# Kernel optimization log

Hardware: AMD Instinct MI355X
Metric: run time of the kernel (lower is better)

## Reference

```python
import jax, jax.numpy as jnp
import numpy as np

B_J0 = 0.01
BETA = 1.8   # isAdapt=1
LENS = 0.5
DT = 1.0
IN_SIZE = 1
STRIDE = IN_SIZE
T = 784 // STRIDE
HID = (512, 512, 512)
OUT = 10
N = 256


def _create_general_mask(dim, c_min, c_max, min_dc, max_dc, phase_max, T):
    # faithful port of ASRNN_general.create_general_mask (numpy, static)
    dcs = np.linspace(min_dc, max_dc, dim)
    cycles = np.linspace(c_min, c_max, dim)
    shifts = np.linspace(0.0, float(int(phase_max * c_max)), dim)
    rows = []
    for cyc, dc, ps in zip(cycles, dcs, shifts):
        cyc = int(np.round(cyc))
        on = int(np.round(dc * cyc))
        pat = [1.0] * on + [0.0] * (cyc - on)
        ps = int(np.round(ps))
        if ps > 0:
            pat = pat[-ps:] + pat[:-ps]
        rows.append(pat * (T // cyc) + pat[: T % cyc])
    return np.asarray(rows, dtype=np.float32)  # [dim, T]

MASK1 = jnp.asarray(_create_general_mask(HID[0], 2, 8, 0.2, 0.8, 0.5, T))
MASK2 = jnp.asarray(_create_general_mask(HID[1], 4, 16, 0.2, 0.8, 0.5, T))
MASK3 = jnp.asarray(_create_general_mask(HID[2], 8, 32, 0.2, 0.8, 0.5, T))

# per-step input gather indices (faithful to the start_idx branch in forward)
_starts = np.arange(T) * STRIDE
_IDX = np.where(_starts[:, None] < T - IN_SIZE,
                _starts[:, None] + np.arange(IN_SIZE)[None, :],
                (784 - IN_SIZE) + np.arange(IN_SIZE)[None, :])  # [T, IN]


@jax.custom_vjp
def act_fun(x):
    return (x > 0.0).astype(x.dtype)

def _act_fwd(x):
    return (x > 0.0).astype(x.dtype), x

def _act_bwd(x, g):
    return (g * (jnp.abs(x) < LENS).astype(g.dtype),)

act_fun.defvjp(_act_fwd, _act_bwd)


def _mem_update(inputs, mem, spike, tau_adp, b, tau_m, mask_t):
    alpha = jnp.exp(-DT / tau_m)
    ro = jnp.exp(-DT / tau_adp)
    b_new = ro * b + (1.0 - ro) * spike
    Bth = B_J0 + BETA * b_new
    mem_new = mem * alpha + (1.0 - alpha) * inputs - Bth * spike * DT
    mem_new = jnp.where(mask_t == 0.0, mem, mem_new)
    spike_new = act_fun(mem_new - Bth) * mask_t
    return mem_new, spike_new, b_new


def _forward(x, wi1, bi1, wh1, bh1, wi2, bi2, wh2, bh2, wi3, bi3, wo, bo,
             tau_adp1, tau_adp2, tau_adp3, tau_m1, tau_m2, tau_m3):
    n = x.shape[0]
    x_seq = jnp.transpose(x[:, _IDX], (1, 0, 2))            # [T, N, IN]
    pre1 = jnp.einsum('tni,hi->tnh', x_seq, wi1) + bi1       # [T, N, H1]

    def step_fn(carry, xs):
        mem1, spk1, b1, mem2, spk2, b2, mem3, spk3, b3, out_sum, s1, s2, s3 = carry
        p1, m1, m2, m3 = xs
        h1_in = p1 + spk1 @ wh1.T + bh1
        mem1, spk1, b1 = _mem_update(h1_in, mem1, spk1, tau_adp1, b1, tau_m1, m1)
        h2_in = spk1 @ wi2.T + bi2 + spk2 @ wh2.T + bh2
        mem2, spk2, b2 = _mem_update(h2_in, mem2, spk2, tau_adp2, b2, tau_m2, m2)
        h3_in = spk2 @ wi3.T + bi3
        mem3, spk3, b3 = _mem_update(h3_in, mem3, spk3, tau_adp3, b3, tau_m3, m3)
        out_sum = out_sum + spk3 @ wo.T + bo
        return (mem1, spk1, b1, mem2, spk2, b2, mem3, spk3, b3,
                out_sum, s1 + spk1, s2 + spk2, s3 + spk3), None

    z = lambda h: jnp.zeros((n, h), x.dtype)
    f = lambda h: jnp.full((n, h), B_J0, x.dtype)
    carry0 = (z(HID[0]), z(HID[0]), f(HID[0]),
              z(HID[1]), z(HID[1]), f(HID[1]),
              z(HID[2]), z(HID[2]), f(HID[2]),
              jnp.zeros((n, OUT), x.dtype), z(HID[0]), z(HID[1]), z(HID[2]))
    xs = (pre1, MASK1.T, MASK2.T, MASK3.T)
    carry, _ = jax.lax.scan(step_fn, carry0, xs)
    out_sum, s1, s2, s3 = carry[9], carry[10], carry[11], carry[12]
    outputs = out_sum / T
    layer_fr = jnp.stack([s1.sum() / (n * HID[0] * T),
                          s2.sum() / (n * HID[1] * T),
                          s3.sum() / (n * HID[2] * T)])
    return outputs, s1 / T, s2 / T, s3 / T, layer_fr


def setup_inputs() -> dict:
    key = jax.random.key(0)
    ks = jax.random.split(key, 20)
    def xav(k, shp):
        fan_in, fan_out = shp[1], shp[0]
        s = np.sqrt(2.0 / (fan_in + fan_out))
        return jax.random.normal(k, shp, jnp.float32) * s
    return {
        'x': jax.random.uniform(ks[0], (N, 784), jnp.float32),
        'wi1': xav(ks[1], (HID[0], IN_SIZE)), 'bi1': jnp.zeros((HID[0],), jnp.float32),
        'wh1': xav(ks[2], (HID[0], HID[0])), 'bh1': jnp.zeros((HID[0],), jnp.float32),
        'wi2': xav(ks[3], (HID[1], HID[0])), 'bi2': jnp.zeros((HID[1],), jnp.float32),
        'wh2': xav(ks[4], (HID[1], HID[1])), 'bh2': jnp.zeros((HID[1],), jnp.float32),
        'wi3': xav(ks[5], (HID[2], HID[1])), 'bi3': jnp.zeros((HID[2],), jnp.float32),
        'wo': xav(ks[6], (OUT, HID[2])), 'bo': jnp.zeros((OUT,), jnp.float32),
        'tau_adp1': 700.0 + 25.0 * jax.random.normal(ks[7], (HID[0],), jnp.float32),
        'tau_adp2': 700.0 + 25.0 * jax.random.normal(ks[8], (HID[1],), jnp.float32),
        'tau_adp3': 700.0 + 25.0 * jax.random.normal(ks[9], (HID[2],), jnp.float32),
        'tau_m1': 5.0 + jax.random.normal(ks[10], (HID[0],), jnp.float32),
        'tau_m2': 5.0 + jax.random.normal(ks[11], (HID[1],), jnp.float32),
        'tau_m3': 5.0 + jax.random.normal(ks[12], (HID[2],), jnp.float32),
    }


def reference(x, wi1, bi1, wh1, bh1, wi2, bi2, wh2, bh2, wi3, bi3, wo, bo,
              tau_adp1, tau_adp2, tau_adp3, tau_m1, tau_m2, tau_m3):
    return _forward(x, wi1, bi1, wh1, bh1, wi2, bi2, wh2, bh2, wi3, bi3, wo, bo,
                    tau_adp1, tau_adp2, tau_adp3, tau_m1, tau_m2, tau_m3)
```

## Files before the change

### kernel.cpp

```cpp
#include <hip/hip_runtime.h>
#include <stdint.h>

#pragma clang fp contract(off)


static constexpr int    TS      = 784;
static constexpr size_t WS_WT1  = 0;
static constexpr size_t WS_WT2A = 1u << 20;
static constexpr size_t WS_WT2B = 2u << 20;
static constexpr size_t WS_WT3  = 3u << 20;
static constexpr size_t WS_M1   = 4u << 20;
static constexpr size_t WS_M2   = WS_M1 + (size_t)TS * 512;
static constexpr size_t WS_M3   = WS_M2 + (size_t)TS * 512;
static constexpr size_t WS_FRP  = WS_M3 + (size_t)TS * 512;

__device__ __forceinline__ float exp_np(float x) {
  float q = rintf(x * 1.442695040f);
  float r = __fmaf_rn(-q, 0.693359375f, x);
  r = __fmaf_rn(-q, -2.12194440e-4f, r);
  float r2 = r * r;
  float p = 1.9875691500e-4f;
  p = __fmaf_rn(p, r, 1.3981999507e-3f);
  p = __fmaf_rn(p, r, 8.3334519073e-3f);
  p = __fmaf_rn(p, r, 4.1665795894e-2f);
  p = __fmaf_rn(p, r, 1.6666665459e-1f);
  p = __fmaf_rn(p, r, 5.0000001201e-1f);
  p = __fmaf_rn(p, r2, r);
  p = p + 1.0f;
  return ldexpf(p, (int)q);
}

__device__ __forceinline__ int mask_val(int l, int h, int t) {
  const double cmin = (l == 0) ? 2.0 : ((l == 1) ? 4.0 : 8.0);
  const double cmax = (l == 0) ? 8.0 : ((l == 1) ? 16.0 : 32.0);
  const double smax = (l == 0) ? 4.0 : ((l == 1) ? 8.0 : 16.0);
  const double cD = (cmax - cmin) / 511.0;
  const double dD = (0.8 - 0.2) / 511.0;
  const double sD = smax / 511.0;
  const double hd = (double)h;
  double cycd = (h == 511) ? cmax : __dadd_rn(cmin, __dmul_rn(hd, cD));
  double dcd  = (h == 511) ? 0.8  : __dadd_rn(0.2,  __dmul_rn(hd, dD));
  double psd  = (h == 511) ? smax : __dmul_rn(hd, sD);
  int cyc = __double2int_rn(cycd);
  int on  = __double2int_rn(__dmul_rn(dcd, (double)cyc));
  int ps  = __double2int_rn(psd);
  int eff = (ps >= cyc) ? 0 : ps;
  int pos = (t % cyc) - eff;
  if (pos < 0) pos += cyc;
  return (pos < on) ? 1 : 0;
}

__global__ void setup_masks(char* __restrict__ ws) {
  const int t = blockIdx.x, tid = threadIdx.x;
  uint8_t* m1 = (uint8_t*)(ws + WS_M1);
  uint8_t* m2 = (uint8_t*)(ws + WS_M2);
  uint8_t* m3 = (uint8_t*)(ws + WS_M3);
  for (int h = tid; h < 512; h += 256) {
    m1[t * 512 + h] = (uint8_t)mask_val(0, h, t);
    m2[t * 512 + h] = (uint8_t)mask_val(1, h, t);
    m3[t * 512 + h] = (uint8_t)mask_val(2, h, t);
  }
}

__global__ void transpose_kernel(const float* __restrict__ wh1,
                                 const float* __restrict__ wi2,
                                 const float* __restrict__ wh2,
                                 const float* __restrict__ wi3,
                                 char* __restrict__ ws) {
  const int k = blockIdx.x;
  const int m = blockIdx.y;
  const float* W = (m == 0) ? wh1 : (m == 1) ? wi2 : (m == 2) ? wh2 : wi3;
  float* T = (float*)(ws + (size_t)m * (1u << 20));
  for (int j = threadIdx.x; j < 512; j += 256)
    T[(size_t)k * 512 + j] = W[(size_t)j * 512 + k];
}

__device__ __forceinline__ uint32_t upd32(float hin, uint32_t mk, uint32_t osp,
                                          float al, float om, float r, float omr,
                                          float& memv, float& bv) {
  float t1 = r * bv;
  float bn = osp ? (t1 + omr) : t1;
  float bt = 1.8f * bn;
  float Bth = 0.01f + bt;
  float m1 = memv * al;
  float m2 = om * hin;
  float m3 = m1 + m2;
  float mn = osp ? (m3 - Bth) : m3;
  if (!mk) mn = memv;
  uint32_t sn = (mk && (mn - Bth) > 0.0f) ? 1u : 0u;
  memv = mn; bv = bn;
  return sn;
}

__device__ __forceinline__ int expand_list(const uint64_t* __restrict__ bm,
                                           uint32_t mysp, int h,
                                           ushort* __restrict__ kl) {
  const int wh = h >> 6, bpos = h & 63;
  int cnt = 0, rank = 0;
#pragma unroll
  for (int w = 0; w < 8; ++w) {
    uint64_t v = bm[w];
    int pc = __builtin_popcountll(v);
    if (w < wh) rank += pc;
    cnt += pc;
  }
  rank += __builtin_popcountll(bm[wh] & ((1ull << bpos) - 1ull));
  if (mysp) kl[rank] = (ushort)h;
  return cnt;
}

__device__ __forceinline__ float gather_from(const float* __restrict__ base,
                                             const ushort* kl, int from, int cnt,
                                             float s) {
  int i = from;
  for (; i + 16 <= cnt; i += 16) {
    float w0  = base[(size_t)kl[i + 0]  << 9];
    float w1  = base[(size_t)kl[i + 1]  << 9];
    float w2  = base[(size_t)kl[i + 2]  << 9];
    float w3  = base[(size_t)kl[i + 3]  << 9];
    float w4  = base[(size_t)kl[i + 4]  << 9];
    float w5  = base[(size_t)kl[i + 5]  << 9];
    float w6  = base[(size_t)kl[i + 6]  << 9];
    float w7  = base[(size_t)kl[i + 7]  << 9];
    float w8  = base[(size_t)kl[i + 8]  << 9];
    float w9  = base[(size_t)kl[i + 9]  << 9];
    float w10 = base[(size_t)kl[i + 10] << 9];
    float w11 = base[(size_t)kl[i + 11] << 9];
    float w12 = base[(size_t)kl[i + 12] << 9];
    float w13 = base[(size_t)kl[i + 13] << 9];
    float w14 = base[(size_t)kl[i + 14] << 9];
    float w15 = base[(size_t)kl[i + 15] << 9];
    s = s + w0;  s = s + w1;  s = s + w2;  s = s + w3;
    s = s + w4;  s = s + w5;  s = s + w6;  s = s + w7;
    s = s + w8;  s = s + w9;  s = s + w10; s = s + w11;
    s = s + w12; s = s + w13; s = s + w14; s = s + w15;
  }
  for (; i + 4 <= cnt; i += 4) {
    float w0 = base[(size_t)kl[i + 0] << 9];
    float w1 = base[(size_t)kl[i + 1] << 9];
    float w2 = base[(size_t)kl[i + 2] << 9];
    float w3 = base[(size_t)kl[i + 3] << 9];
    s = s + w0; s = s + w1; s = s + w2; s = s + w3;
  }
  for (; i < cnt; ++i) s = s + base[(size_t)kl[i] << 9];
  return s;
}

__device__ __forceinline__ void dual_gather(
    const float* __restrict__ bA, const ushort* __restrict__ klA, int cntA,
    const float* __restrict__ bB, const ushort* __restrict__ klB, int cntB,
    float& outA, float& outB) {
  float a = 0.0f, b = 0.0f;
  int iA = 0, iB = 0;
  while (iA + 8 <= cntA && iB + 8 <= cntB) {
    float wa0 = bA[(size_t)klA[iA + 0] << 9];
    float wa1 = bA[(size_t)klA[iA + 1] << 9];
    float wa2 = bA[(size_t)klA[iA + 2] << 9];
    float wa3 = bA[(size_t)klA[iA + 3] << 9];
    float wa4 = bA[(size_t)klA[iA + 4] << 9];
    float wa5 = bA[(size_t)klA[iA + 5] << 9];
    float wa6 = bA[(size_t)klA[iA + 6] << 9];
    float wa7 = bA[(size_t)klA[iA + 7] << 9];
    float wb0 = bB[(size_t)klB[iB + 0] << 9];
    float wb1 = bB[(size_t)klB[iB + 1] << 9];
    float wb2 = bB[(size_t)klB[iB + 2] << 9];
    float wb3 = bB[(size_t)klB[iB + 3] << 9];
    float wb4 = bB[(size_t)klB[iB + 4] << 9];
    float wb5 = bB[(size_t)klB[iB + 5] << 9];
    float wb6 = bB[(size_t)klB[iB + 6] << 9];
    float wb7 = bB[(size_t)klB[iB + 7] << 9];
    a = a + wa0; a = a + wa1; a = a + wa2; a = a + wa3;
    a = a + wa4; a = a + wa5; a = a + wa6; a = a + wa7;
    b = b + wb0; b = b + wb1; b = b + wb2; b = b + wb3;
    b = b + wb4; b = b + wb5; b = b + wb6; b = b + wb7;
    iA += 8; iB += 8;
  }
  a = gather_from(bA, klA, iA, cntA, a);
  b = gather_from(bB, klB, iB, cntB, b);
  outA = a; outB = b;
}

__global__ __launch_bounds__(512, 1) void rnn_block(
    const float* __restrict__ x,
    const float* __restrict__ wi1, const float* __restrict__ bi1,
    const float* __restrict__ bh1,
    const float* __restrict__ bi2, const float* __restrict__ bh2,
    const float* __restrict__ bi3,
    const float* __restrict__ wo, const float* __restrict__ bo,
    const float* __restrict__ ta1, const float* __restrict__ ta2,
    const float* __restrict__ ta3, const float* __restrict__ tm1,
    const float* __restrict__ tm2, const float* __restrict__ tm3,
    char* __restrict__ ws, float* __restrict__ d_out) {
  const int n = blockIdx.x;
  const int h = threadIdx.x;
  const float* WT1  = (const float*)(ws + WS_WT1);
  const float* WT2A = (const float*)(ws + WS_WT2A);
  const float* WT2B = (const float*)(ws + WS_WT2B);
  const float* WT3  = (const float*)(ws + WS_WT3);
  const uint8_t* M1 = (const uint8_t*)(ws + WS_M1);
  const uint8_t* M2 = (const uint8_t*)(ws + WS_M2);
  const uint8_t* M3 = (const uint8_t*)(ws + WS_M3);

  __shared__ uint64_t bm1s[8], bm2s[8];
  __shared__ ushort kl1s[512], kl2s[512];
  __shared__ float outpS[512 * 10];
  __shared__ double red[512];

  float al1 = exp_np(-1.0f / tm1[h]), om1 = 1.0f - al1;
  float ro1 = exp_np(-1.0f / ta1[h]), omr1 = 1.0f - ro1;
  float al2 = exp_np(-1.0f / tm2[h]), om2 = 1.0f - al2;
  float ro2 = exp_np(-1.0f / ta2[h]), omr2 = 1.0f - ro2;
  float al3 = exp_np(-1.0f / tm3[h]), om3 = 1.0f - al3;
  float ro3 = exp_np(-1.0f / ta3[h]), omr3 = 1.0f - ro3;
  float wi1v = wi1[h], bi1v = bi1[h], bh1v = bh1[h];
  float bi2v = bi2[h], bh2v = bh2[h], bi3v = bi3[h];

  float wov[10], outp[10];
#pragma unroll
  for (int o = 0; o < 10; ++o) { wov[o] = wo[(size_t)o * 512 + h]; outp[o] = 0.0f; }

  float mem1 = 0.0f, b1 = 0.01f, c1 = 0.0f;
  float mem2 = 0.0f, b2 = 0.01f, c2 = 0.0f;
  float mem3 = 0.0f, b3 = 0.01f, c3 = 0.0f;
  uint32_t sp1 = 0, sp2 = 0, sp3 = 0;
  int cnt1 = 0, cnt2 = 0;
  float acc1 = 0.0f;
  uint32_t mk1 = M1[h];

  const float* xrow = x + (size_t)n * 784;
  __syncthreads();

  for (int t = 0; t < TS; ++t) {
    const uint32_t mk2 = M2[t * 512 + h];
    const uint32_t mk3 = M3[t * 512 + h];
    const float xv = xrow[t];

    float p1 = xv * wi1v;
    p1 = p1 + bi1v;
    p1 = p1 + acc1;
    p1 = p1 + bh1v;
    uint32_t sn1 = upd32(p1, mk1, sp1, al1, om1, ro1, omr1, mem1, b1);
    sp1 = sn1; c1 += (float)sn1;
    uint64_t bal1 = __ballot(sn1);
    if ((h & 63) == 0) bm1s[h >> 6] = bal1;
    __syncthreads();
    cnt1 = expand_list(bm1s, sn1, h, kl1s);
    __syncthreads();

    float a1, a2;
    {
      const int cA = mk2 ? cnt1 : 0;
      const int cB = mk2 ? cnt2 : 0;
      dual_gather(WT2A + h, kl1s, cA, WT2B + h, kl2s, cB, a1, a2);
    }
    float p2 = a1 + bi2v;
    p2 = p2 + a2;
    p2 = p2 + bh2v;
    uint32_t sn2 = upd32(p2, mk2, sp2, al2, om2, ro2, omr2, mem2, b2);
    sp2 = sn2; c2 += (float)sn2;
    uint64_t bal2 = __ballot(sn2);
    if ((h & 63) == 0) bm2s[h >> 6] = bal2;
    __syncthreads();
    cnt2 = expand_list(bm2s, sn2, h, kl2s);
    __syncthreads();

    const uint32_t mk1n = (t + 1 < TS) ? M1[(t + 1) * 512 + h] : 0u;
    float a3, a1n;
    {
      const int cG3 = mk3 ? cnt2 : 0;
      const int cG1 = mk1n ? cnt1 : 0;
      dual_gather(WT3 + h, kl2s, cG3, WT1 + h, kl1s, cG1, a3, a1n);
    }
    acc1 = a1n;
    mk1 = mk1n;
    float p3 = a3 + bi3v;
    uint32_t sn3 = upd32(p3, mk3, sp3, al3, om3, ro3, omr3, mem3, b3);
    sp3 = sn3; c3 += (float)sn3;

    if (sn3) {
#pragma unroll
      for (int o = 0; o < 10; ++o) outp[o] = outp[o] + wov[o];
    }
  }

  d_out[2560 + (size_t)n * 512 + h]          = c1 / 784.0f;
  d_out[2560 + 131072 + (size_t)n * 512 + h] = c2 / 784.0f;
  d_out[2560 + 262144 + (size_t)n * 512 + h] = c3 / 784.0f;

#pragma unroll
  for (int o = 0; o < 10; ++o) outpS[h * 10 + o] = outp[o];
  __syncthreads();
  if (h < 10) {
    double s = 0.0;
    for (int l = 0; l < 512; ++l) s += (double)outpS[l * 10 + h];
    s += 784.0 * (double)bo[h];
    d_out[(size_t)n * 10 + h] = (float)s / 784.0f;
  }

  double* FRP = (double*)(ws + WS_FRP);
  red[h] = (double)c1;
  __syncthreads();
  for (int wd = 256; wd > 0; wd >>= 1) {
    if (h < wd) red[h] += red[h + wd];
    __syncthreads();
  }
  if (h == 0) FRP[n * 3 + 0] = red[0];
  __syncthreads();
  red[h] = (double)c2;
  __syncthreads();
  for (int wd = 256; wd > 0; wd >>= 1) {
    if (h < wd) red[h] += red[h + wd];
    __syncthreads();
  }
  if (h == 0) FRP[n * 3 + 1] = red[0];
  __syncthreads();
  red[h] = (double)c3;
  __syncthreads();
  for (int wd = 256; wd > 0; wd >>= 1) {
    if (h < wd) red[h] += red[h + wd];
    __syncthreads();
  }
  if (h == 0) FRP[n * 3 + 2] = red[0];
}

__global__ void finalize_fr(char* __restrict__ ws, float* __restrict__ d_out) {
  const int l = threadIdx.x;
  if (l >= 3) return;
  const double* FRP = (const double*)(ws + WS_FRP);
  double s = 0.0;
  for (int n = 0; n < 256; ++n) s += FRP[n * 3 + l];
  d_out[395776 + l] = (float)(s / (131072.0 * 784.0));
}

extern "C" void kernel_launch(void* const* d_in, const int* in_sizes, int n_in,
                              void* d_out, int out_size, void* d_ws, size_t ws_size,
                              hipStream_t stream) {
  (void)in_sizes; (void)n_in; (void)out_size; (void)ws_size;
  const float* x   = (const float*)d_in[0];
  const float* wi1 = (const float*)d_in[1];
  const float* bi1 = (const float*)d_in[2];
  const float* wh1 = (const float*)d_in[3];
  const float* bh1 = (const float*)d_in[4];
  const float* wi2 = (const float*)d_in[5];
  const float* bi2 = (const float*)d_in[6];
  const float* wh2 = (const float*)d_in[7];
  const float* bh2 = (const float*)d_in[8];
  const float* wi3 = (const float*)d_in[9];
  const float* bi3 = (const float*)d_in[10];
  const float* wo  = (const float*)d_in[11];
  const float* bo  = (const float*)d_in[12];
  const float* ta1 = (const float*)d_in[13];
  const float* ta2 = (const float*)d_in[14];
  const float* ta3 = (const float*)d_in[15];
  const float* tm1 = (const float*)d_in[16];
  const float* tm2 = (const float*)d_in[17];
  const float* tm3 = (const float*)d_in[18];
  char*  ws  = (char*)d_ws;
  float* out = (float*)d_out;

  hipLaunchKernelGGL(setup_masks, dim3(TS), dim3(256), 0, stream, ws);
  hipLaunchKernelGGL(transpose_kernel, dim3(512, 4), dim3(256), 0, stream,
                     wh1, wi2, wh2, wi3, ws);
  hipLaunchKernelGGL(rnn_block, dim3(256), dim3(512), 0, stream,
                     x, wi1, bi1, bh1, bi2, bh2, bi3, wo, bo,
                     ta1, ta2, ta3, tm1, tm2, tm3, ws, out);
  hipLaunchKernelGGL(finalize_fr, dim3(1), dim3(64), 0, stream, ws, out);
}
```

Baseline: 4.301 ms.

## Permute neurons by mask pattern so warps share mask phase

Adds a permutation kernel that sorts each layer's neurons by their mask cycle, phase and duty parameters, then assigns threads to neurons in that sorted order. Masks and transposed weights are stored in permuted order, and spikes are scattered through shared memory to rebuild bitmaps and gather lists in each layer's permuted index space. The goal is for whole wavefronts to share mask state, so masked-off wavefronts skip gathers uniformly and divergence drops. In exchange each layer step gets an extra shared-memory scatter and barrier, plus a small setup kernel.

```diff
diff --git a/kernel.cpp b/kernel.cpp
--- a/kernel.cpp
+++ b/kernel.cpp
@@ -13,6 +13,7 @@
 static constexpr size_t WS_M2   = WS_M1 + (size_t)TS * 512;
 static constexpr size_t WS_M3   = WS_M2 + (size_t)TS * 512;
 static constexpr size_t WS_FRP  = WS_M3 + (size_t)TS * 512;
+static constexpr size_t WS_PRM  = WS_FRP + 256 * 3 * 8;
 
 __device__ __forceinline__ float exp_np(float x) {
   float q = rintf(x * 1.442695040f);
@@ -50,15 +51,48 @@
   return (pos < on) ? 1 : 0;
 }
 
+__global__ void perm_kernel(char* __restrict__ ws) {
+  const int tid = threadIdx.x;
+  __shared__ int keys[512];
+  int* PRM = (int*)(ws + WS_PRM);
+  for (int l = 0; l < 3; ++l) {
+    const double cmin = (l == 0) ? 2.0 : ((l == 1) ? 4.0 : 8.0);
+    const double cmax = (l == 0) ? 8.0 : ((l == 1) ? 16.0 : 32.0);
+    const double smax = (l == 0) ? 4.0 : ((l == 1) ? 8.0 : 16.0);
+    const double cD = (cmax - cmin) / 511.0;
+    const double dD = (0.8 - 0.2) / 511.0;
+    const double sD = smax / 511.0;
+    const double hd = (double)tid;
+    double cycd = (tid == 511) ? cmax : __dadd_rn(cmin, __dmul_rn(hd, cD));
+    double dcd  = (tid == 511) ? 0.8  : __dadd_rn(0.2,  __dmul_rn(hd, dD));
+    double psd  = (tid == 511) ? smax : __dmul_rn(hd, sD);
+    int cyc = __double2int_rn(cycd);
+    int on  = __double2int_rn(__dmul_rn(dcd, (double)cyc));
+    int ps  = __double2int_rn(psd);
+    int eff = (ps >= cyc) ? 0 : ps;
+    int key = cyc * 2048 + eff * 64 + on;
+    keys[tid] = key;
+    __syncthreads();
+    int rank = 0;
+    for (int h2 = 0; h2 < 512; ++h2) {
+      int k2 = keys[h2];
+      rank += (k2 < key) || (k2 == key && h2 < tid);
+    }
+    PRM[l * 512 + rank] = tid;
+    __syncthreads();
+  }
+}
+
 __global__ void setup_masks(char* __restrict__ ws) {
   const int t = blockIdx.x, tid = threadIdx.x;
+  const int* PRM = (const int*)(ws + WS_PRM);
   uint8_t* m1 = (uint8_t*)(ws + WS_M1);
   uint8_t* m2 = (uint8_t*)(ws + WS_M2);
   uint8_t* m3 = (uint8_t*)(ws + WS_M3);
-  for (int h = tid; h < 512; h += 256) {
-    m1[t * 512 + h] = (uint8_t)mask_val(0, h, t);
-    m2[t * 512 + h] = (uint8_t)mask_val(1, h, t);
-    m3[t * 512 + h] = (uint8_t)mask_val(2, h, t);
+  for (int i = tid; i < 512; i += 256) {
+    m1[t * 512 + i] = (uint8_t)mask_val(0, PRM[i], t);
+    m2[t * 512 + i] = (uint8_t)mask_val(1, PRM[512 + i], t);
+    m3[t * 512 + i] = (uint8_t)mask_val(2, PRM[1024 + i], t);
   }
 }
 
@@ -69,10 +103,12 @@
                                  char* __restrict__ ws) {
   const int k = blockIdx.x;
   const int m = blockIdx.y;
+  const int* PRM = (const int*)(ws + WS_PRM);
   const float* W = (m == 0) ? wh1 : (m == 1) ? wi2 : (m == 2) ? wh2 : wi3;
+  const int* pp = (m == 0) ? PRM : (m == 3) ? (PRM + 1024) : (PRM + 512);
   float* T = (float*)(ws + (size_t)m * (1u << 20));
   for (int j = threadIdx.x; j < 512; j += 256)
-    T[(size_t)k * 512 + j] = W[(size_t)j * 512 + k];
+    T[(size_t)k * 512 + j] = W[(size_t)pp[j] * 512 + k];
 }
 
 __device__ __forceinline__ uint32_t upd32(float hin, uint32_t mk, uint32_t osp,
@@ -93,9 +129,9 @@
 }
 
 __device__ __forceinline__ int expand_list(const uint64_t* __restrict__ bm,
-                                           uint32_t mysp, int h,
+                                           uint32_t mysp, int kidx,
                                            ushort* __restrict__ kl) {
-  const int wh = h >> 6, bpos = h & 63;
+  const int wh = kidx >> 6, bpos = kidx & 63;
   int cnt = 0, rank = 0;
 #pragma unroll
   for (int w = 0; w < 8; ++w) {
@@ -105,7 +141,7 @@
     cnt += pc;
   }
   rank += __builtin_popcountll(bm[wh] & ((1ull << bpos) - 1ull));
-  if (mysp) kl[rank] = (ushort)h;
+  if (mysp) kl[rank] = (ushort)kidx;
   return cnt;
 }
 
@@ -191,8 +227,8 @@
     const float* __restrict__ ta3, const float* __restrict__ tm1,
     const float* __restrict__ tm2, const float* __restrict__ tm3,
     char* __restrict__ ws, float* __restrict__ d_out) {
-  const int n = blockIdx.x;
-  const int h = threadIdx.x;
+  const int n   = blockIdx.x;
+  const int tid = threadIdx.x;
   const float* WT1  = (const float*)(ws + WS_WT1);
   const float* WT2A = (const float*)(ws + WS_WT2A);
   const float* WT2B = (const float*)(ws + WS_WT2B);
@@ -200,24 +236,30 @@
   const uint8_t* M1 = (const uint8_t*)(ws + WS_M1);
   const uint8_t* M2 = (const uint8_t*)(ws + WS_M2);
   const uint8_t* M3 = (const uint8_t*)(ws + WS_M3);
-
-  __shared__ uint64_t bm1s[8], bm2s[8];
+  const int* PRM = (const int*)(ws + WS_PRM);
+
+  __shared__ uint64_t bmk1[8], bmk2[8];
   __shared__ ushort kl1s[512], kl2s[512];
+  __shared__ uint8_t sby1[512], sby2[512];
   __shared__ float outpS[512 * 10];
   __shared__ double red[512];
 
-  float al1 = exp_np(-1.0f / tm1[h]), om1 = 1.0f - al1;
-  float ro1 = exp_np(-1.0f / ta1[h]), omr1 = 1.0f - ro1;
-  float al2 = exp_np(-1.0f / tm2[h]), om2 = 1.0f - al2;
-  float ro2 = exp_np(-1.0f / ta2[h]), omr2 = 1.0f - ro2;
-  float al3 = exp_np(-1.0f / tm3[h]), om3 = 1.0f - al3;
-  float ro3 = exp_np(-1.0f / ta3[h]), omr3 = 1.0f - ro3;
-  float wi1v = wi1[h], bi1v = bi1[h], bh1v = bh1[h];
-  float bi2v = bi2[h], bh2v = bh2[h], bi3v = bi3[h];
+  const int h1 = PRM[tid];
+  const int h2 = PRM[512 + tid];
+  const int h3 = PRM[1024 + tid];
+
+  float al1 = exp_np(-1.0f / tm1[h1]), om1 = 1.0f - al1;
+  float ro1 = exp_np(-1.0f / ta1[h1]), omr1 = 1.0f - ro1;
+  float al2 = exp_np(-1.0f / tm2[h2]), om2 = 1.0f - al2;
+  float ro2 = exp_np(-1.0f / ta2[h2]), omr2 = 1.0f - ro2;
+  float al3 = exp_np(-1.0f / tm3[h3]), om3 = 1.0f - al3;
+  float ro3 = exp_np(-1.0f / ta3[h3]), omr3 = 1.0f - ro3;
+  float wi1v = wi1[h1], bi1v = bi1[h1], bh1v = bh1[h1];
+  float bi2v = bi2[h2], bh2v = bh2[h2], bi3v = bi3[h3];
 
   float wov[10], outp[10];
 #pragma unroll
-  for (int o = 0; o < 10; ++o) { wov[o] = wo[(size_t)o * 512 + h]; outp[o] = 0.0f; }
+  for (int o = 0; o < 10; ++o) { wov[o] = wo[(size_t)o * 512 + h3]; outp[o] = 0.0f; }
 
   float mem1 = 0.0f, b1 = 0.01f, c1 = 0.0f;
   float mem2 = 0.0f, b2 = 0.01f, c2 = 0.0f;
@@ -225,14 +267,14 @@
   uint32_t sp1 = 0, sp2 = 0, sp3 = 0;
   int cnt1 = 0, cnt2 = 0;
   float acc1 = 0.0f;
-  uint32_t mk1 = M1[h];
+  uint32_t mk1 = M1[tid];
 
   const float* xrow = x + (size_t)n * 784;
   __syncthreads();
 
   for (int t = 0; t < TS; ++t) {
-    const uint32_t mk2 = M2[t * 512 + h];
-    const uint32_t mk3 = M3[t * 512 + h];
+    const uint32_t mk2 = M2[t * 512 + tid];
+    const uint32_t mk3 = M3[t * 512 + tid];
     const float xv = xrow[t];
 
     float p1 = xv * wi1v;
@@ -241,35 +283,41 @@
     p1 = p1 + bh1v;
     uint32_t sn1 = upd32(p1, mk1, sp1, al1, om1, ro1, omr1, mem1, b1);
     sp1 = sn1; c1 += (float)sn1;
-    uint64_t bal1 = __ballot(sn1);
-    if ((h & 63) == 0) bm1s[h >> 6] = bal1;
-    __syncthreads();
-    cnt1 = expand_list(bm1s, sn1, h, kl1s);
+    sby1[h1] = (uint8_t)sn1;
+    __syncthreads();
+    uint32_t bv1 = sby1[tid];
+    uint64_t balk1 = __ballot(bv1);
+    if ((tid & 63) == 0) bmk1[tid >> 6] = balk1;
+    __syncthreads();
+    cnt1 = expand_list(bmk1, bv1, tid, kl1s);
     __syncthreads();
 
     float a1, a2;
     {
       const int cA = mk2 ? cnt1 : 0;
       const int cB = mk2 ? cnt2 : 0;
-      dual_gather(WT2A + h, kl1s, cA, WT2B + h, kl2s, cB, a1, a2);
+      dual_gather(WT2A + tid, kl1s, cA, WT2B + tid, kl2s, cB, a1, a2);
     }
     float p2 = a1 + bi2v;
     p2 = p2 + a2;
     p2 = p2 + bh2v;
     uint32_t sn2 = upd32(p2, mk2, sp2, al2, om2, ro2, omr2, mem2, b2);
     sp2 = sn2; c2 += (float)sn2;
-    uint64_t bal2 = __ballot(sn2);
-    if ((h & 63) == 0) bm2s[h >> 6] = bal2;
-    __syncthreads();
-    cnt2 = expand_list(bm2s, sn2, h, kl2s);
-    __syncthreads();
-
-    const uint32_t mk1n = (t + 1 < TS) ? M1[(t + 1) * 512 + h] : 0u;
+    sby2[h2] = (uint8_t)sn2;
+    __syncthreads();
+    uint32_t bv2 = sby2[tid];
+    uint64_t balk2 = __ballot(bv2);
+    if ((tid & 63) == 0) bmk2[tid >> 6] = balk2;
+    __syncthreads();
+    cnt2 = expand_list(bmk2, bv2, tid, kl2s);
+    __syncthreads();
+
+    const uint32_t mk1n = (t + 1 < TS) ? M1[(t + 1) * 512 + tid] : 0u;
     float a3, a1n;
     {
       const int cG3 = mk3 ? cnt2 : 0;
       const int cG1 = mk1n ? cnt1 : 0;
-      dual_gather(WT3 + h, kl2s, cG3, WT1 + h, kl1s, cG1, a3, a1n);
+      dual_gather(WT3 + tid, kl2s, cG3, WT1 + tid, kl1s, cG1, a3, a1n);
     }
     acc1 = a1n;
     mk1 = mk1n;
@@ -283,44 +331,44 @@
     }
   }
 
-  d_out[2560 + (size_t)n * 512 + h]          = c1 / 784.0f;
-  d_out[2560 + 131072 + (size_t)n * 512 + h] = c2 / 784.0f;
-  d_out[2560 + 262144 + (size_t)n * 512 + h] = c3 / 784.0f;
+  d_out[2560 + (size_t)n * 512 + h1]          = c1 / 784.0f;
+  d_out[2560 + 131072 + (size_t)n * 512 + h2] = c2 / 784.0f;
+  d_out[2560 + 262144 + (size_t)n * 512 + h3] = c3 / 784.0f;
 
 #pragma unroll
-  for (int o = 0; o < 10; ++o) outpS[h * 10 + o] = outp[o];
-  __syncthreads();
-  if (h < 10) {
+  for (int o = 0; o < 10; ++o) outpS[tid * 10 + o] = outp[o];
+  __syncthreads();
+  if (tid < 10) {
     double s = 0.0;
-    for (int l = 0; l < 512; ++l) s += (double)outpS[l * 10 + h];
-    s += 784.0 * (double)bo[h];
-    d_out[(size_t)n * 10 + h] = (float)s / 784.0f;
+    for (int l = 0; l < 512; ++l) s += (double)outpS[l * 10 + tid];
+    s += 784.0 * (double)bo[tid];
+    d_out[(size_t)n * 10 + tid] = (float)s / 784.0f;
   }
 
   double* FRP = (double*)(ws + WS_FRP);
-  red[h] = (double)c1;
+  red[tid] = (double)c1;
   __syncthreads();
   for (int wd = 256; wd > 0; wd >>= 1) {
-    if (h < wd) red[h] += red[h + wd];
-    __syncthreads();
-  }
-  if (h == 0) FRP[n * 3 + 0] = red[0];
-  __syncthreads();
-  red[h] = (double)c2;
+    if (tid < wd) red[tid] += red[tid + wd];
+    __syncthreads();
+  }
+  if (tid == 0) FRP[n * 3 + 0] = red[0];
+  __syncthreads();
+  red[tid] = (double)c2;
   __syncthreads();
   for (int wd = 256; wd > 0; wd >>= 1) {
-    if (h < wd) red[h] += red[h + wd];
-    __syncthreads();
-  }
-  if (h == 0) FRP[n * 3 + 1] = red[0];
-  __syncthreads();
-  red[h] = (double)c3;
+    if (tid < wd) red[tid] += red[tid + wd];
+    __syncthreads();
+  }
+  if (tid == 0) FRP[n * 3 + 1] = red[0];
+  __syncthreads();
+  red[tid] = (double)c3;
   __syncthreads();
   for (int wd = 256; wd > 0; wd >>= 1) {
-    if (h < wd) red[h] += red[h + wd];
-    __syncthreads();
-  }
-  if (h == 0) FRP[n * 3 + 2] = red[0];
+    if (tid < wd) red[tid] += red[tid + wd];
+    __syncthreads();
+  }
+  if (tid == 0) FRP[n * 3 + 2] = red[0];
 }
 
 __global__ void finalize_fr(char* __restrict__ ws, float* __restrict__ d_out) {
@@ -358,6 +406,7 @@
   char*  ws  = (char*)d_ws;
   float* out = (float*)d_out;
 
+  hipLaunchKernelGGL(perm_kernel, dim3(1), dim3(512), 0, stream, ws);
   hipLaunchKernelGGL(setup_masks, dim3(TS), dim3(256), 0, stream, ws);
   hipLaunchKernelGGL(transpose_kernel, dim3(512, 4), dim3(256), 0, stream,
                      wh1, wi2, wh2, wi3, ws);
```

Result: slower. 4.390 ms (+2.1%).
